# Kernel optimization log

Hardware: AMD Instinct MI355X
Metric: run time of the kernel (lower is better)

Reference implementation:

```python
import jax, jax.numpy as jnp
import numpy as np

B, T, DIM = 2, 2048, 1024
H, HKV, D = 16, 4, 64
ROPE_DIMS = 32
ROPE_BASE = 10000.0


def fake_quant(w, n_bits):
    # per-output-row absmax symmetric fake quantization with STE
    half = 2 ** (n_bits - 1)
    w_max = jnp.maximum(jnp.max(jnp.abs(w), axis=1, keepdims=True), 1e-5)
    w_int = jnp.clip(jnp.round(w / w_max * half), -half, half - 1)
    w_q = w_int / half * w_max
    return w + jax.lax.stop_gradient(w_q - w)


def rms_norm(x):
    eps = jnp.finfo(x.dtype).eps
    return x * jax.lax.rsqrt(jnp.mean(x * x, axis=-1, keepdims=True) + eps)


def rope_tables(seq_len, dtype):
    inv_freq = 1.0 / (ROPE_BASE ** (jnp.arange(0, ROPE_DIMS, 2, dtype=jnp.float32) / ROPE_DIMS))
    t = jnp.arange(seq_len, dtype=jnp.float32)
    freqs = t[:, None] * inv_freq[None, :]  # [T, rope_dims/2]
    return jnp.cos(freqs).astype(dtype)[None, None], jnp.sin(freqs).astype(dtype)[None, None]


def apply_rotary(x, cos, sin):
    # partial rotary: rotate first ROPE_DIMS dims, pass the rest through
    x_rope, x_pass = x[..., :ROPE_DIMS], x[..., ROPE_DIMS:]
    half = ROPE_DIMS // 2
    x1, x2 = x_rope[..., :half], x_rope[..., half:]
    rot = jnp.concatenate([x1 * cos + x2 * sin, -x1 * sin + x2 * cos], axis=-1)
    return jnp.concatenate([rot, x_pass], axis=-1)


def setup_inputs() -> dict:
    key = jax.random.key(0)
    ks = jax.random.split(key, 5)
    kv_dim = HKV * D
    return {
        "x": jax.random.normal(ks[0], (B, T, DIM), dtype=jnp.float32),
        "w_q": jax.random.normal(ks[1], (DIM, DIM), dtype=jnp.float32) * 0.02,
        "w_k": jax.random.normal(ks[2], (kv_dim, DIM), dtype=jnp.float32) * 0.02,
        "w_v": jax.random.normal(ks[3], (kv_dim, DIM), dtype=jnp.float32) * 0.02,
        "w_proj": jax.random.normal(ks[4], (DIM, DIM), dtype=jnp.float32) * 0.02,
        "q_gain": jnp.full((H,), 1.5, dtype=jnp.float32),
    }


def reference(x, w_q, w_k, w_v, w_proj, q_gain):
    bsz, seqlen, dim = x.shape
    group = H // HKV

    # quantized (STE) projections
    q = x @ fake_quant(w_q, 6).T        # [B, T, DIM]
    k = x @ fake_quant(w_k, 6).T        # [B, T, HKV*D]
    v = x @ fake_quant(w_v, 5).T        # [B, T, HKV*D]

    q = q.reshape(bsz, seqlen, H, D).transpose(0, 2, 1, 3)    # [B, H, T, D]
    k = k.reshape(bsz, seqlen, HKV, D).transpose(0, 2, 1, 3)  # [B, HKV, T, D]
    v = v.reshape(bsz, seqlen, HKV, D).transpose(0, 2, 1, 3)  # [B, HKV, T, D]

    q = rms_norm(q)
    k = rms_norm(k)

    cos, sin = rope_tables(seqlen, q.dtype)
    q = apply_rotary(q, cos, sin)
    k = apply_rotary(k, cos, sin)

    q = q * q_gain.astype(q.dtype)[None, :, None, None]

    # grouped-query causal attention; scores kept in grouped [B,HKV,g,T,T] layout
    qg = q.reshape(bsz, HKV, group, seqlen, D)
    scores = jnp.einsum('bhgqd,bhkd->bhgqk', qg, k) / jnp.sqrt(jnp.asarray(D, q.dtype))
    causal = jnp.tril(jnp.ones((seqlen, seqlen), dtype=bool))
    scores = jnp.where(causal[None, None, None], scores, jnp.asarray(-jnp.inf, scores.dtype))
    att = jax.nn.softmax(scores, axis=-1)
    y = jnp.einsum('bhgqk,bhkd->bhgqd', att, v)               # [B, HKV, g, T, D]

    # xsa: orthogonalize y against normalized v (per kv head group)
    y_g = y.transpose(0, 3, 1, 2, 4)                           # [B, T, HKV, g, D]
    v_t = v.transpose(0, 2, 1, 3)                              # [B, T, HKV, D]
    vn = v_t / jnp.maximum(jnp.linalg.norm(v_t, axis=-1, keepdims=True), 1e-12)
    vn = vn[..., None, :]                                      # [B, T, HKV, 1, D]
    proj = jnp.sum(y_g * vn, axis=-1, keepdims=True) * vn
    y_out = (y_g - proj).reshape(bsz, seqlen, dim)

    return y_out @ fake_quant(w_proj, 5).T
```

## Files before the change

kernel.cpp:

```cpp
#include <hip/hip_runtime.h>
#include <math.h>

typedef unsigned short u16;
typedef __attribute__((ext_vector_type(8))) short short8;
typedef __attribute__((ext_vector_type(4))) float float4v;
typedef __attribute__((ext_vector_type(4))) u16 ushort4v;

namespace {
constexpr int kT    = 2048;
constexpr int kDim  = 1024;
constexpr int kH    = 16;
constexpr int kHKV  = 4;
constexpr int kD    = 64;
constexpr int kTok  = 4096;
constexpr int kQKVN = 1536;
}

__device__ __forceinline__ u16 f2bf(float f) {
  unsigned int u = __builtin_bit_cast(unsigned int, f);
  u = (u + 0x7FFFu + ((u >> 16) & 1u)) >> 16;
  return (u16)u;
}

__global__ __launch_bounds__(256) void prep_kernel(
    const float* __restrict__ x,
    const float* __restrict__ w_q, const float* __restrict__ w_k,
    const float* __restrict__ w_v, const float* __restrict__ w_proj,
    u16* __restrict__ xb, u16* __restrict__ wqkv, u16* __restrict__ wpq,
    float2* __restrict__ ropetab)
{
  __shared__ float red[4];
  const int bid = blockIdx.x, tid = threadIdx.x;

  if (bid < 128) {
    const int idx = bid * 256 + tid;
    const int t = idx >> 4, i = idx & 15;
    const float fr = (float)t * powf(10000.0f, -(float)i * (1.0f / 16.0f));
    ropetab[idx] = make_float2(cosf(fr), sinf(fr));
    return;
  }
  if (bid < 2176) {
    const size_t i = ((size_t)(bid - 128) * 256 + tid) * 8;
    const float4 a = *(const float4*)(x + i);
    const float4 b = *(const float4*)(x + i + 4);
    short8 r;
    r[0] = (short)f2bf(a.x); r[1] = (short)f2bf(a.y);
    r[2] = (short)f2bf(a.z); r[3] = (short)f2bf(a.w);
    r[4] = (short)f2bf(b.x); r[5] = (short)f2bf(b.y);
    r[6] = (short)f2bf(b.z); r[7] = (short)f2bf(b.w);
    *(short8*)(xb + i) = r;
    return;
  }
  const int rid = bid - 2176;
  const float* src; u16* dst; float halfv;
  if (rid < 1024)      { src = w_q    + (size_t)rid * 1024;          dst = wqkv + (size_t)rid * 1024;          halfv = 32.0f; }
  else if (rid < 1280) { src = w_k    + (size_t)(rid - 1024) * 1024; dst = wqkv + (size_t)rid * 1024;          halfv = 32.0f; }
  else if (rid < 1536) { src = w_v    + (size_t)(rid - 1280) * 1024; dst = wqkv + (size_t)rid * 1024;          halfv = 16.0f; }
  else                 { src = w_proj + (size_t)(rid - 1536) * 1024; dst = wpq  + (size_t)(rid - 1536) * 1024; halfv = 16.0f; }

  const float4 v4 = *(const float4*)(src + tid * 4);
  float mx = fmaxf(fmaxf(fabsf(v4.x), fabsf(v4.y)), fmaxf(fabsf(v4.z), fabsf(v4.w)));
  #pragma unroll
  for (int m = 1; m < 64; m <<= 1) mx = fmaxf(mx, __shfl_xor(mx, m));
  if ((tid & 63) == 0) red[tid >> 6] = mx;
  __syncthreads();
  mx = fmaxf(fmaxf(red[0], red[1]), fmaxf(red[2], red[3]));
  const float wmax = fmaxf(mx, 1e-5f);
  const float inv_half = 1.0f / halfv;
  const float vals[4] = {v4.x, v4.y, v4.z, v4.w};
  ushort4v o;
  #pragma unroll
  for (int j = 0; j < 4; ++j) {
    float r = rintf(vals[j] / wmax * halfv);
    r = fminf(fmaxf(r, -halfv), halfv - 1.0f);
    o[j] = f2bf(r * inv_half * wmax);
  }
  *(ushort4v*)(dst + tid * 4) = o;
}

#define GEMM_CORE(A_, W_, K_, NCOL0_)                                          \
  __shared__ u16 As[128][32];                                                  \
  __shared__ u16 Bs[64][32];                                                   \
  const int tid = threadIdx.x;                                                 \
  const int lane = tid & 63, wv = tid >> 6;                                    \
  const int n = lane & 15, quad = lane >> 4;                                   \
  const int wm = wv * 32;                                                      \
  const int m0 = blockIdx.y * 128;                                             \
  const int sr = tid >> 2, sc = (tid & 3) * 8;                                 \
  const int scs = sc ^ ((sr & 3) * 8);                                         \
  float4v acc[2][4];                                                           \
  _Pragma("unroll")                                                            \
  for (int mi = 0; mi < 2; ++mi)                                               \
    _Pragma("unroll")                                                          \
    for (int ni = 0; ni < 4; ++ni) {                                           \
      acc[mi][ni][0]=0.f; acc[mi][ni][1]=0.f;                                  \
      acc[mi][ni][2]=0.f; acc[mi][ni][3]=0.f; }                                \
  short8 a0r, a1r, b0r;                                                        \
  a0r = *(const short8*)(A_ + (size_t)(m0 + sr) * K_ + sc);                    \
  a1r = *(const short8*)(A_ + (size_t)(m0 + sr + 64) * K_ + sc);               \
  b0r = *(const short8*)(W_ + (size_t)(NCOL0_ + sr) * K_ + sc);                \
  for (int k0 = 0; k0 < K_; k0 += 32) {                                        \
    __syncthreads();                                                           \
    *(short8*)&As[sr][scs] = a0r;  *(short8*)&As[sr + 64][scs] = a1r;          \
    *(short8*)&Bs[sr][scs] = b0r;                                              \
    __syncthreads();                                                           \
    if (k0 + 32 < K_) {                                                        \
      a0r = *(const short8*)(A_ + (size_t)(m0 + sr) * K_ + k0 + 32 + sc);      \
      a1r = *(const short8*)(A_ + (size_t)(m0 + sr + 64) * K_ + k0 + 32 + sc); \
      b0r = *(const short8*)(W_ + (size_t)(NCOL0_ + sr) * K_ + k0 + 32 + sc);  \
    }                                                                          \
    short8 af[2], bf[4];                                                       \
    _Pragma("unroll")                                                          \
    for (int mi = 0; mi < 2; ++mi)                                             \
      af[mi] = *(const short8*)&As[wm + mi * 16 + n][(quad * 8) ^ ((n & 3) * 8)]; \
    _Pragma("unroll")                                                          \
    for (int ni = 0; ni < 4; ++ni)                                             \
      bf[ni] = *(const short8*)&Bs[ni * 16 + n][(quad * 8) ^ ((n & 3) * 8)];   \
    _Pragma("unroll")                                                          \
    for (int mi = 0; mi < 2; ++mi)                                             \
      _Pragma("unroll")                                                        \
      for (int ni = 0; ni < 4; ++ni)                                           \
        acc[mi][ni] = __builtin_amdgcn_mfma_f32_16x16x32_bf16(af[mi], bf[ni], acc[mi][ni], 0, 0, 0); \
  }

__global__ __launch_bounds__(256) void gemm_qkv(
    const u16* __restrict__ A, const u16* __restrict__ W,
    const float2* __restrict__ ropetab, const float* __restrict__ q_gain,
    u16* __restrict__ qh, u16* __restrict__ kh,
    u16* __restrict__ vT, float* __restrict__ vcmp)
{
  GEMM_CORE(A, W, kDim, (int)(blockIdx.x * 64))

  const int p = blockIdx.x;
  const int rbase = m0 + wm;
  const int bI = rbase >> 11;

  if (p < 20) {
    const float gain = (p < 16) ? q_gain[p] * 0.125f : 1.0f;
    u16* dst = (p < 16) ? qh + ((size_t)(bI * kH + p) * kT) * kD
                        : kh + ((size_t)(bI * kHKV + (p - 16)) * kT) * kD;
    #pragma unroll
    for (int mi = 0; mi < 2; ++mi)
      #pragma unroll
      for (int i = 0; i < 4; ++i) {
        const int row = rbase + mi * 16 + quad * 4 + i;
        const int t = row & (kT - 1);
        float v[4];
        #pragma unroll
        for (int ni = 0; ni < 4; ++ni) v[ni] = acc[mi][ni][i];
        float ss = v[0]*v[0] + v[1]*v[1] + v[2]*v[2] + v[3]*v[3];
        #pragma unroll
        for (int m = 1; m < 16; m <<= 1) ss += __shfl_xor(ss, m);
        const float rr = 1.0f / sqrtf(ss * (1.0f / 64.0f) + 1.1920929e-7f);
        #pragma unroll
        for (int ni = 0; ni < 4; ++ni) v[ni] *= rr;
        const float2 cs = ropetab[t * 16 + n];
        const float r0 =  v[0] * cs.x + v[1] * cs.y;
        const float r1 = -v[0] * cs.y + v[1] * cs.x;
        v[0] = r0; v[1] = r1;
        #pragma unroll
        for (int ni = 0; ni < 4; ++ni)
          dst[(size_t)t * kD + ni * 16 + n] = f2bf(v[ni] * gain);
      }
  } else {
    const int kvh = p - 20;
    u16* vTb = vT + ((size_t)(bI * kHKV + kvh) * kD) * kT;
    #pragma unroll
    for (int mi = 0; mi < 2; ++mi) {
      const int t0 = (rbase + mi * 16 + quad * 4) & (kT - 1);
      #pragma unroll
      for (int ni = 0; ni < 4; ++ni) {
        const int d = ni * 16 + n;
        ushort4v pk;
        pk[0] = f2bf(acc[mi][ni][0]); pk[1] = f2bf(acc[mi][ni][1]);
        pk[2] = f2bf(acc[mi][ni][2]); pk[3] = f2bf(acc[mi][ni][3]);
        *(ushort4v*)(vTb + (size_t)d * kT + t0) = pk;
        #pragma unroll
        for (int i = 0; i < 4; ++i)
          vcmp[(size_t)(rbase + mi * 16 + quad * 4 + i) * (kHKV * kD) + kvh * kD + d] = acc[mi][ni][i];
      }
    }
  }
}

__global__ __launch_bounds__(256) void gemm_out(
    const u16* __restrict__ A, const u16* __restrict__ W,
    float* __restrict__ C)
{
  GEMM_CORE(A, W, kDim, (int)(blockIdx.x * 64))
  const int n0 = blockIdx.x * 64;
  #pragma unroll
  for (int mi = 0; mi < 2; ++mi)
    #pragma unroll
    for (int ni = 0; ni < 4; ++ni)
      #pragma unroll
      for (int i = 0; i < 4; ++i)
        C[(size_t)(m0 + wm + mi * 16 + quad * 4 + i) * kDim + n0 + ni * 16 + n] = acc[mi][ni][i];
}

__global__ __launch_bounds__(256) void attn_mfma(
    const u16* __restrict__ qh, const u16* __restrict__ kh,
    const u16* __restrict__ vT, const float* __restrict__ vcmp,
    u16* __restrict__ yo)
{
  __shared__ u16 ks[64][64];
  __shared__ u16 vs[64][64];
  __shared__ u16 ps[4][16][64];

  const int tid = threadIdx.x;
  const int lane = tid & 63, wq = tid >> 6;
  const int n = lane & 15, quad = lane >> 4;
  const int p = blockIdx.x;
  const int h = blockIdx.y, b = blockIdx.z;
  const int kv = h >> 2;
  const int tiles[2] = {p, 31 - p};
  const u16* kbase = kh + ((size_t)(b * kHKV + kv) * kT) * kD;
  const u16* vbase = vT + ((size_t)(b * kHKV + kv) * kD) * kT;

  short8 qa[2][2];
  {
    const u16* qb = qh + ((size_t)(b * kH + h) * kT) * kD;
    #pragma unroll
    for (int u = 0; u < 2; ++u) {
      const size_t row = (size_t)(tiles[u] * 64 + wq * 16 + n) * kD;
      qa[u][0] = *(const short8*)(qb + row + quad * 8);
      qa[u][1] = *(const short8*)(qb + row + 32 + quad * 8);
    }
  }

  const int sr = tid >> 3;
  const int sc = (tid & 7) * 8;
  const int scs = sc ^ ((sr & 7) * 8);

  float l_r[2] = {0.0f, 0.0f};
  float4v acc[2][4];
  #pragma unroll
  for (int u = 0; u < 2; ++u)
    #pragma unroll
    for (int g = 0; g < 4; ++g) { acc[u][g][0]=0.f; acc[u][g][1]=0.f; acc[u][g][2]=0.f; acc[u][g][3]=0.f; }

  short8 kr0, kr1, vr0, vr1;
  auto loadKV = [&](int kt) {
    kr0 = *(const short8*)(kbase + (size_t)(kt * 64 + sr) * kD + sc);
    kr1 = *(const short8*)(kbase + (size_t)(kt * 64 + sr + 32) * kD + sc);
    vr0 = *(const short8*)(vbase + (size_t)sr * kT + kt * 64 + sc);
    vr1 = *(const short8*)(vbase + (size_t)(sr + 32) * kT + kt * 64 + sc);
  };

  auto process = [&](int u, int kt) {
    float4v s[4];
    #pragma unroll
    for (int g = 0; g < 4; ++g) { s[g][0]=0.f; s[g][1]=0.f; s[g][2]=0.f; s[g][3]=0.f; }
    #pragma unroll
    for (int g = 0; g < 4; ++g) {
      const short8 kb0 = *(const short8*)&ks[g * 16 + n][(quad * 8) ^ ((n & 7) * 8)];
      s[g] = __builtin_amdgcn_mfma_f32_16x16x32_bf16(kb0, qa[u][0], s[g], 0, 0, 0);
      const short8 kb1 = *(const short8*)&ks[g * 16 + n][(32 + quad * 8) ^ ((n & 7) * 8)];
      s[g] = __builtin_amdgcn_mfma_f32_16x16x32_bf16(kb1, qa[u][1], s[g], 0, 0, 0);
    }
    if (kt == tiles[u]) {
      const int mloc = wq * 16 + n;
      #pragma unroll
      for (int g = 0; g < 4; ++g)
        #pragma unroll
        for (int i = 0; i < 4; ++i)
          if (g * 16 + quad * 4 + i > mloc) s[g][i] = -__builtin_inff();
    }
    float pf[4][4]; float rs = 0.0f;
    #pragma unroll
    for (int g = 0; g < 4; ++g)
      #pragma unroll
      for (int i = 0; i < 4; ++i) { pf[g][i] = __expf(s[g][i] - 12.0f); rs += pf[g][i]; }
    rs += __shfl_xor(rs, 16);
    rs += __shfl_xor(rs, 32);
    l_r[u] += rs;
    #pragma unroll
    for (int g = 0; g < 4; ++g) {
      ushort4v pk;
      pk[0] = f2bf(pf[g][0]); pk[1] = f2bf(pf[g][1]);
      pk[2] = f2bf(pf[g][2]); pk[3] = f2bf(pf[g][3]);
      *(ushort4v*)&ps[wq][n][(g * 16 + quad * 4) ^ ((n & 7) * 8)] = pk;
    }
    const short8 pb0 = *(const short8*)&ps[wq][n][(quad * 8) ^ ((n & 7) * 8)];
    const short8 pb1 = *(const short8*)&ps[wq][n][(32 + quad * 8) ^ ((n & 7) * 8)];
    #pragma unroll
    for (int g = 0; g < 4; ++g) {
      const short8 vb0 = *(const short8*)&vs[g * 16 + n][(quad * 8) ^ ((n & 7) * 8)];
      acc[u][g] = __builtin_amdgcn_mfma_f32_16x16x32_bf16(vb0, pb0, acc[u][g], 0, 0, 0);
      const short8 vb1 = *(const short8*)&vs[g * 16 + n][(32 + quad * 8) ^ ((n & 7) * 8)];
      acc[u][g] = __builtin_amdgcn_mfma_f32_16x16x32_bf16(vb1, pb1, acc[u][g], 0, 0, 0);
    }
  };

  const int kmax = tiles[1];
  loadKV(0);
  for (int kt = 0; kt <= kmax; ++kt) {
    __syncthreads();
    *(short8*)&ks[sr][scs]      = kr0;
    *(short8*)&ks[sr + 32][scs] = kr1;
    *(short8*)&vs[sr][scs]      = vr0;
    *(short8*)&vs[sr + 32][scs] = vr1;
    __syncthreads();
    if (kt < kmax) loadKV(kt + 1);
    process(1, kt);
    if (kt <= tiles[0]) process(0, kt);
  }

  #pragma unroll
  for (int u = 0; u < 2; ++u) {
    const int tok = b * kT + tiles[u] * 64 + wq * 16 + n;
    const float invl = 1.0f / l_r[u];
    float4 vv[4]; float nn = 0.0f, syr = 0.0f;
    #pragma unroll
    for (int g = 0; g < 4; ++g) {
      vv[g] = *(const float4*)(vcmp + (size_t)tok * (kHKV * kD) + kv * kD + g * 16 + quad * 4);
      nn  += vv[g].x * vv[g].x + vv[g].y * vv[g].y + vv[g].z * vv[g].z + vv[g].w * vv[g].w;
      syr += acc[u][g][0] * vv[g].x + acc[u][g][1] * vv[g].y + acc[u][g][2] * vv[g].z + acc[u][g][3] * vv[g].w;
    }
    nn  += __shfl_xor(nn, 16);  nn  += __shfl_xor(nn, 32);
    syr += __shfl_xor(syr, 16); syr += __shfl_xor(syr, 32);
    const float inv = 1.0f / fmaxf(sqrtf(nn), 1e-12f);
    const float coef = syr * invl * inv * inv;
    #pragma unroll
    for (int g = 0; g < 4; ++g) {
      const float vf[4] = {vv[g].x, vv[g].y, vv[g].z, vv[g].w};
      ushort4v ow;
      #pragma unroll
      for (int i = 0; i < 4; ++i)
        ow[i] = f2bf(acc[u][g][i] * invl - coef * vf[i]);
      *(ushort4v*)(yo + (size_t)tok * kDim + h * kD + g * 16 + quad * 4) = ow;
    }
  }
}

extern "C" void kernel_launch(void* const* d_in, const int* in_sizes, int n_in,
                              void* d_out, int out_size, void* d_ws, size_t ws_size,
                              hipStream_t stream) {
  (void)in_sizes; (void)n_in; (void)out_size; (void)ws_size;
  const float* x      = (const float*)d_in[0];
  const float* w_q    = (const float*)d_in[1];
  const float* w_k    = (const float*)d_in[2];
  const float* w_v    = (const float*)d_in[3];
  const float* w_proj = (const float*)d_in[4];
  const float* q_gain = (const float*)d_in[5];

  char* wsb = (char*)d_ws;
  u16* wqkv = (u16*)wsb;  wsb += (size_t)1536 * 1024 * 2;
  u16* wpq  = (u16*)wsb;  wsb += (size_t)1024 * 1024 * 2;
  u16* xb   = (u16*)wsb;  wsb += (size_t)kTok * kDim * 2;
  u16* qh   = (u16*)wsb;  wsb += (size_t)kTok * kDim * 2;
  u16* khb  = (u16*)wsb;  wsb += (size_t)kTok * kHKV * kD * 2;
  u16* vTb  = (u16*)wsb;  wsb += (size_t)kTok * kHKV * kD * 2;
  u16* yo   = (u16*)wsb;  wsb += (size_t)kTok * kDim * 2;
  float* vcmp = (float*)wsb; wsb += (size_t)kTok * kHKV * kD * 4;
  float2* ropetab = (float2*)wsb; wsb += (size_t)kT * 16 * sizeof(float2);

  prep_kernel<<<4736, 256, 0, stream>>>(x, w_q, w_k, w_v, w_proj,
                                        xb, wqkv, wpq, ropetab);

  gemm_qkv<<<dim3(24, 32), 256, 0, stream>>>(xb, wqkv, ropetab, q_gain,
                                             qh, khb, vTb, vcmp);

  attn_mfma<<<dim3(16, kH, 2), 256, 0, stream>>>(qh, khb, vTb, vcmp, yo);

  gemm_out<<<dim3(16, 32), 256, 0, stream>>>(yo, wpq, (float*)d_out);
}
```

Measured before the change: 165.3 us.

## Enlarge GEMM tiles to 128x128 and load tiles via global_load_lds

Both projection GEMMs now use a 128x128 output tile per block, with each wave computing a 64x64 sub-tile. The extra reuse per LDS load is meant to raise arithmetic intensity. Global-to-LDS copies go through the direct global_load_lds builtin instead of staging in registers. This drops the register prefetch and the XOR swizzle, so LDS bank conflicts may increase and global loads no longer overlap with compute. The grids halve, leaving fewer blocks (384 and 256) to fill the CUs.

```diff
diff --git a/kernel.cpp b/kernel.cpp
--- a/kernel.cpp
+++ b/kernel.cpp
@@ -20,6 +20,12 @@
   unsigned int u = __builtin_bit_cast(unsigned int, f);
   u = (u + 0x7FFFu + ((u >> 16) & 1u)) >> 16;
   return (u16)u;
+}
+
+__device__ __forceinline__ void gload_lds16(const u16* g, u16* l) {
+  __builtin_amdgcn_global_load_lds(
+      (const __attribute__((address_space(1))) void*)g,
+      (__attribute__((address_space(3))) void*)l, 16, 0, 0);
 }
 
 __global__ __launch_bounds__(256) void prep_kernel(
@@ -78,46 +84,42 @@
   *(ushort4v*)(dst + tid * 4) = o;
 }
 
-#define GEMM_CORE(A_, W_, K_, NCOL0_)                                          \
+#define GEMM_CORE128(A_, W_, K_, N0_)                                          \
   __shared__ u16 As[128][32];                                                  \
-  __shared__ u16 Bs[64][32];                                                   \
+  __shared__ u16 Bs[128][32];                                                  \
   const int tid = threadIdx.x;                                                 \
   const int lane = tid & 63, wv = tid >> 6;                                    \
   const int n = lane & 15, quad = lane >> 4;                                   \
-  const int wm = wv * 32;                                                      \
+  const int wrow = (wv >> 1) * 64, wcol = (wv & 1) * 64;                       \
   const int m0 = blockIdx.y * 128;                                             \
-  const int sr = tid >> 2, sc = (tid & 3) * 8;                                 \
-  const int scs = sc ^ ((sr & 3) * 8);                                         \
-  float4v acc[2][4];                                                           \
+  const int lr = tid >> 2, lc = (tid & 3) * 8;                                 \
+  const u16* agp0 = A_ + (size_t)(m0 + lr) * K_ + lc;                          \
+  const u16* agp1 = agp0 + (size_t)64 * K_;                                    \
+  const u16* bgp0 = W_ + (size_t)(N0_ + lr) * K_ + lc;                         \
+  const u16* bgp1 = bgp0 + (size_t)64 * K_;                                    \
+  float4v acc[4][4];                                                           \
   _Pragma("unroll")                                                            \
-  for (int mi = 0; mi < 2; ++mi)                                               \
+  for (int mi = 0; mi < 4; ++mi)                                               \
     _Pragma("unroll")                                                          \
     for (int ni = 0; ni < 4; ++ni) {                                           \
       acc[mi][ni][0]=0.f; acc[mi][ni][1]=0.f;                                  \
       acc[mi][ni][2]=0.f; acc[mi][ni][3]=0.f; }                                \
-  short8 a0r, a1r, b0r;                                                        \
-  a0r = *(const short8*)(A_ + (size_t)(m0 + sr) * K_ + sc);                    \
-  a1r = *(const short8*)(A_ + (size_t)(m0 + sr + 64) * K_ + sc);               \
-  b0r = *(const short8*)(W_ + (size_t)(NCOL0_ + sr) * K_ + sc);                \
   for (int k0 = 0; k0 < K_; k0 += 32) {                                        \
     __syncthreads();                                                           \
-    *(short8*)&As[sr][scs] = a0r;  *(short8*)&As[sr + 64][scs] = a1r;          \
-    *(short8*)&Bs[sr][scs] = b0r;                                              \
+    gload_lds16(agp0 + k0, &As[lr][lc]);                                       \
+    gload_lds16(agp1 + k0, &As[64 + lr][lc]);                                  \
+    gload_lds16(bgp0 + k0, &Bs[lr][lc]);                                       \
+    gload_lds16(bgp1 + k0, &Bs[64 + lr][lc]);                                  \
     __syncthreads();                                                           \
-    if (k0 + 32 < K_) {                                                        \
-      a0r = *(const short8*)(A_ + (size_t)(m0 + sr) * K_ + k0 + 32 + sc);      \
-      a1r = *(const short8*)(A_ + (size_t)(m0 + sr + 64) * K_ + k0 + 32 + sc); \
-      b0r = *(const short8*)(W_ + (size_t)(NCOL0_ + sr) * K_ + k0 + 32 + sc);  \
-    }                                                                          \
-    short8 af[2], bf[4];                                                       \
+    short8 af[4], bf[4];                                                       \
     _Pragma("unroll")                                                          \
-    for (int mi = 0; mi < 2; ++mi)                                             \
-      af[mi] = *(const short8*)&As[wm + mi * 16 + n][(quad * 8) ^ ((n & 3) * 8)]; \
+    for (int mi = 0; mi < 4; ++mi)                                             \
+      af[mi] = *(const short8*)&As[wrow + mi * 16 + n][quad * 8];              \
     _Pragma("unroll")                                                          \
     for (int ni = 0; ni < 4; ++ni)                                             \
-      bf[ni] = *(const short8*)&Bs[ni * 16 + n][(quad * 8) ^ ((n & 3) * 8)];   \
+      bf[ni] = *(const short8*)&Bs[wcol + ni * 16 + n][quad * 8];              \
     _Pragma("unroll")                                                          \
-    for (int mi = 0; mi < 2; ++mi)                                             \
+    for (int mi = 0; mi < 4; ++mi)                                             \
       _Pragma("unroll")                                                        \
       for (int ni = 0; ni < 4; ++ni)                                           \
         acc[mi][ni] = __builtin_amdgcn_mfma_f32_16x16x32_bf16(af[mi], bf[ni], acc[mi][ni], 0, 0, 0); \
@@ -129,10 +131,10 @@
     u16* __restrict__ qh, u16* __restrict__ kh,
     u16* __restrict__ vT, float* __restrict__ vcmp)
 {
-  GEMM_CORE(A, W, kDim, (int)(blockIdx.x * 64))
-
-  const int p = blockIdx.x;
-  const int rbase = m0 + wm;
+  GEMM_CORE128(A, W, kDim, (int)(blockIdx.x * 128))
+
+  const int p = blockIdx.x * 2 + (wv & 1);
+  const int rbase = m0 + wrow;
   const int bI = rbase >> 11;
 
   if (p < 20) {
@@ -140,7 +142,7 @@
     u16* dst = (p < 16) ? qh + ((size_t)(bI * kH + p) * kT) * kD
                         : kh + ((size_t)(bI * kHKV + (p - 16)) * kT) * kD;
     #pragma unroll
-    for (int mi = 0; mi < 2; ++mi)
+    for (int mi = 0; mi < 4; ++mi)
       #pragma unroll
       for (int i = 0; i < 4; ++i) {
         const int row = rbase + mi * 16 + quad * 4 + i;
@@ -166,7 +168,7 @@
     const int kvh = p - 20;
     u16* vTb = vT + ((size_t)(bI * kHKV + kvh) * kD) * kT;
     #pragma unroll
-    for (int mi = 0; mi < 2; ++mi) {
+    for (int mi = 0; mi < 4; ++mi) {
       const int t0 = (rbase + mi * 16 + quad * 4) & (kT - 1);
       #pragma unroll
       for (int ni = 0; ni < 4; ++ni) {
@@ -187,15 +189,15 @@
     const u16* __restrict__ A, const u16* __restrict__ W,
     float* __restrict__ C)
 {
-  GEMM_CORE(A, W, kDim, (int)(blockIdx.x * 64))
-  const int n0 = blockIdx.x * 64;
-  #pragma unroll
-  for (int mi = 0; mi < 2; ++mi)
+  GEMM_CORE128(A, W, kDim, (int)(blockIdx.x * 128))
+  const int c0 = blockIdx.x * 128 + wcol;
+  #pragma unroll
+  for (int mi = 0; mi < 4; ++mi)
     #pragma unroll
     for (int ni = 0; ni < 4; ++ni)
       #pragma unroll
       for (int i = 0; i < 4; ++i)
-        C[(size_t)(m0 + wm + mi * 16 + quad * 4 + i) * kDim + n0 + ni * 16 + n] = acc[mi][ni][i];
+        C[(size_t)(m0 + wrow + mi * 16 + quad * 4 + i) * kDim + c0 + ni * 16 + n] = acc[mi][ni][i];
 }
 
 __global__ __launch_bounds__(256) void attn_mfma(
@@ -358,10 +360,10 @@
   prep_kernel<<<4736, 256, 0, stream>>>(x, w_q, w_k, w_v, w_proj,
                                         xb, wqkv, wpq, ropetab);
 
-  gemm_qkv<<<dim3(24, 32), 256, 0, stream>>>(xb, wqkv, ropetab, q_gain,
+  gemm_qkv<<<dim3(12, 32), 256, 0, stream>>>(xb, wqkv, ropetab, q_gain,
                                              qh, khb, vTb, vcmp);
 
   attn_mfma<<<dim3(16, kH, 2), 256, 0, stream>>>(qh, khb, vTb, vcmp, yo);
 
-  gemm_out<<<dim3(16, 32), 256, 0, stream>>>(yo, wpq, (float*)d_out);
-}
+  gemm_out<<<dim3(8, 32), 256, 0, stream>>>(yo, wpq, (float*)d_out);
+}
```

After: 178.9 us. 8.2% more time.
